# Performance work log

Hardware: AMD Instinct MI355X
Metric: run time of the kernel (lower is better)

## Reference

```python
import jax, jax.numpy as jnp
from jax import lax
import numpy as np

# Straight-through sign (matches SignActivation: >=0 -> +1, <0 -> -1; identity grad)
@jax.custom_vjp
def binarize(x):
    return jnp.where(x >= 0, 1.0, -1.0).astype(x.dtype)

def _bin_fwd(x):
    return binarize(x), None

def _bin_bwd(_, g):
    return (g,)

binarize.defvjp(_bin_fwd, _bin_bwd)

def binary_tanh(x):
    # BinaryTanh: sign(tanh(x) * 2); grad flows through tanh*2 via STE
    return binarize(jnp.tanh(x) * 2)

def conv2d(x, w, b):
    out = lax.conv_general_dilated(x, w, (1, 1), [(1, 1), (1, 1)],
                                   dimension_numbers=('NCHW', 'OIHW', 'NCHW'))
    return out + b[None, :, None, None]

def bn2d(x, g, b, eps=1e-4):
    # training-mode BatchNorm2d: batch stats over (N,H,W), biased variance
    m = jnp.mean(x, axis=(0, 2, 3), keepdims=True)
    v = jnp.mean(jnp.square(x - m), axis=(0, 2, 3), keepdims=True)
    return g[None, :, None, None] * (x - m) * lax.rsqrt(v + eps) + b[None, :, None, None]

def bn1d(x, g, b, eps=1e-5):
    m = jnp.mean(x, axis=0, keepdims=True)
    v = jnp.mean(jnp.square(x - m), axis=0, keepdims=True)
    return g[None, :] * (x - m) * lax.rsqrt(v + eps) + b[None, :]

def maxpool2(x):
    return lax.reduce_window(x, -jnp.inf, lax.max, (1, 1, 2, 2), (1, 1, 2, 2), 'VALID')

def forward(x, w1, b1, g1, be1, w2, b2, g2, be2, w3, b3, g3, be3,
            w4, b4, g4, be4, w5, b5, g5, be5, w6, b6, g6, be6,
            fcw, fcb, g7, be7):
    # block 1 (32x32)
    x = binary_tanh(bn2d(conv2d(x, w1, b1), g1, be1))           # fp conv 3->64
    x = binary_tanh(bn2d(conv2d(x, binarize(w2), b2), g2, be2))  # bin conv 64->64
    x = maxpool2(x)                                              # 16x16
    # block 2
    x = binary_tanh(bn2d(conv2d(x, binarize(w3), b3), g3, be3))  # 64->128
    x = binary_tanh(bn2d(conv2d(x, binarize(w4), b4), g4, be4))  # 128->128
    x = maxpool2(x)                                              # 8x8
    # block 3
    x = binary_tanh(bn2d(conv2d(x, binarize(w5), b5), g5, be5))  # 128->256
    x = binary_tanh(bn2d(conv2d(x, binarize(w6), b6), g6, be6))  # 256->256
    x = maxpool2(x)                                              # 4x4
    x = jnp.mean(x, axis=(2, 3))                                 # AvgPool2d(4) -> [B,256]
    x = x @ binarize(fcw).T + fcb[None, :]                       # BinaryLinear 256->10
    return bn1d(x, g7, be7)

def setup_inputs() -> dict:
    key = jax.random.key(0)
    ks = jax.random.split(key, 32)
    s = 0.05
    d = {
        'x':  jax.random.normal(ks[0], (512, 3, 32, 32), jnp.float32),
        'w1': jax.random.normal(ks[1], (64, 3, 3, 3), jnp.float32) * s,
        'b1': jax.random.normal(ks[2], (64,), jnp.float32) * s,
        'g1': jnp.ones((64,), jnp.float32),  'be1': jnp.zeros((64,), jnp.float32),
        'w2': jax.random.normal(ks[3], (64, 64, 3, 3), jnp.float32) * s,
        'b2': jax.random.normal(ks[4], (64,), jnp.float32) * s,
        'g2': jnp.ones((64,), jnp.float32),  'be2': jnp.zeros((64,), jnp.float32),
        'w3': jax.random.normal(ks[5], (128, 64, 3, 3), jnp.float32) * s,
        'b3': jax.random.normal(ks[6], (128,), jnp.float32) * s,
        'g3': jnp.ones((128,), jnp.float32), 'be3': jnp.zeros((128,), jnp.float32),
        'w4': jax.random.normal(ks[7], (128, 128, 3, 3), jnp.float32) * s,
        'b4': jax.random.normal(ks[8], (128,), jnp.float32) * s,
        'g4': jnp.ones((128,), jnp.float32), 'be4': jnp.zeros((128,), jnp.float32),
        'w5': jax.random.normal(ks[9], (256, 128, 3, 3), jnp.float32) * s,
        'b5': jax.random.normal(ks[10], (256,), jnp.float32) * s,
        'g5': jnp.ones((256,), jnp.float32), 'be5': jnp.zeros((256,), jnp.float32),
        'w6': jax.random.normal(ks[11], (256, 256, 3, 3), jnp.float32) * s,
        'b6': jax.random.normal(ks[12], (256,), jnp.float32) * s,
        'g6': jnp.ones((256,), jnp.float32), 'be6': jnp.zeros((256,), jnp.float32),
        'fcw': jax.random.normal(ks[13], (10, 256), jnp.float32) * s,
        'fcb': jax.random.normal(ks[14], (10,), jnp.float32) * s,
        'g7': jnp.ones((10,), jnp.float32),  'be7': jnp.zeros((10,), jnp.float32),
    }
    return d

def reference(x, w1, b1, g1, be1, w2, b2, g2, be2, w3, b3, g3, be3,
              w4, b4, g4, be4, w5, b5, g5, be5, w6, b6, g6, be6,
              fcw, fcb, g7, be7):
    return forward(x, w1, b1, g1, be1, w2, b2, g2, be2, w3, b3, g3, be3,
                   w4, b4, g4, be4, w5, b5, g5, be5, w6, b6, g6, be6,
                   fcw, fcb, g7, be7)
```

## Files before the change

kernel.cpp:

```cpp
#include <hip/hip_runtime.h>
#include <cstdint>


typedef int v4i __attribute__((ext_vector_type(4)));
typedef int v16i __attribute__((ext_vector_type(16)));

#define NBKT 256
#define SSTR 1664

__global__ void __launch_bounds__(256) pack8(const float* __restrict__ w2,
                                             const float* __restrict__ w3,
                                             const float* __restrict__ w4,
                                             const float* __restrict__ w5,
                                             const float* __restrict__ w6,
                                             int8_t* __restrict__ w8) {
  const int idx = blockIdx.x * 256 + threadIdx.x;
  const float* w; int CiL, e; int8_t* dst;
  if (idx < 36864)        { w = w2; CiL = 64;  e = idx;          dst = w8; }
  else if (idx < 110592)  { w = w3; CiL = 64;  e = idx - 36864;  dst = w8 + 36864; }
  else if (idx < 258048)  { w = w4; CiL = 128; e = idx - 110592; dst = w8 + 110592; }
  else if (idx < 552960)  { w = w5; CiL = 128; e = idx - 258048; dst = w8 + 258048; }
  else if (idx < 1142784) { w = w6; CiL = 256; e = idx - 552960; dst = w8 + 552960; }
  else return;
  const int WDk = CiL / 32;
  const int b = e & 15;
  const int l31 = (e >> 4) & 31;
  const int hi = (e >> 9) & 1;
  const int kc = (e >> 10) % WDk;
  const int tap = (e / (1024 * WDk)) % 9;
  const int cb = e / (9216 * WDk);
  const int co = cb * 32 + l31;
  const int ci = kc * 32 + hi * 16 + b;
  dst[e] = (w[((size_t)co * CiL + ci) * 9 + tap] >= 0.f) ? (int8_t)1 : (int8_t)-1;
}

__global__ void __launch_bounds__(256, 6) conv1_p1(const float* __restrict__ x,
                                                   const float* __restrict__ w1,
                                                   double2* __restrict__ part) {
  __shared__ float ximg[3][34][34];
  __shared__ float wl[16][28];
  __shared__ double pS[16][4], pQ[16][4];
  const int tid = threadIdx.x, n = blockIdx.x, cg = blockIdx.y;
  for (int i = tid; i < 3 * 34 * 34; i += 256) ((float*)ximg)[i] = 0.f;
  for (int i = tid; i < 16 * 27; i += 256) wl[i / 27][i % 27] = w1[cg * 432 + i];
  __syncthreads();
  const float* xb = x + (size_t)n * 3072;
  for (int i = tid; i < 3072; i += 256) {
    const int c = i >> 10, p = i & 1023;
    ximg[c][(p >> 5) + 1][(p & 31) + 1] = xb[i];
  }
  __syncthreads();
  const int h = tid >> 3, w0 = (tid & 7) * 4;
  const int lane = tid & 63, wv = tid >> 6;
  for (int c = 0; c < 16; c += 2) {
    float4 wa4[7], wb4[7];
#pragma unroll
    for (int i = 0; i < 7; i++) {
      wa4[i] = *(const float4*)&wl[c][i * 4];
      wb4[i] = *(const float4*)&wl[c + 1][i * 4];
    }
    const float* wfa = (const float*)wa4;
    const float* wfb = (const float*)wb4;
    float accA[4] = {0.f, 0.f, 0.f, 0.f};
    float accB[4] = {0.f, 0.f, 0.f, 0.f};
#pragma unroll
    for (int ic = 0; ic < 3; ic++)
#pragma unroll
      for (int ky = 0; ky < 3; ky++) {
        float xr[6];
#pragma unroll
        for (int t = 0; t < 6; t++) xr[t] = ximg[ic][h + ky][w0 + t];
#pragma unroll
        for (int kx = 0; kx < 3; kx++) {
          const float wga = wfa[ic * 9 + ky * 3 + kx];
          const float wgb = wfb[ic * 9 + ky * 3 + kx];
#pragma unroll
          for (int j = 0; j < 4; j++) {
            accA[j] = fmaf(xr[j + kx], wga, accA[j]);
            accB[j] = fmaf(xr[j + kx], wgb, accB[j]);
          }
        }
      }
    double s = (double)accA[0] + accA[1] + accA[2] + accA[3];
    double q = (double)accA[0] * accA[0] + (double)accA[1] * accA[1] +
               (double)accA[2] * accA[2] + (double)accA[3] * accA[3];
    double s2 = (double)accB[0] + accB[1] + accB[2] + accB[3];
    double q2 = (double)accB[0] * accB[0] + (double)accB[1] * accB[1] +
                (double)accB[2] * accB[2] + (double)accB[3] * accB[3];
#pragma unroll
    for (int off = 32; off; off >>= 1) {
      s += __shfl_down(s, off);
      q += __shfl_down(q, off);
      s2 += __shfl_down(s2, off);
      q2 += __shfl_down(q2, off);
    }
    if (lane == 0) {
      pS[c][wv] = s;      pQ[c][wv] = q;
      pS[c + 1][wv] = s2; pQ[c + 1][wv] = q2;
    }
  }
  __syncthreads();
  if (tid < 16) {
    const double S = pS[tid][0] + pS[tid][1] + pS[tid][2] + pS[tid][3];
    const double Q = pQ[tid][0] + pQ[tid][1] + pQ[tid][2] + pQ[tid][3];
    part[(size_t)(cg * 16 + tid) * 512 + n] = make_double2(S, Q);
  }
}

__global__ void __launch_bounds__(256) conv1_fin(const double2* __restrict__ part,
                                                 const float* __restrict__ g,
                                                 const float* __restrict__ be,
                                                 const float* __restrict__ w1,
                                                 double2* __restrict__ thr,
                                                 double* __restrict__ te) {
  __shared__ double sS[4], sQ[4];
  const int c = blockIdx.x;
  const int t = threadIdx.x;
  const double2 a = part[(size_t)c * 512 + t];
  const double2 b = part[(size_t)c * 512 + 256 + t];
  double S = a.x + b.x, Q = a.y + b.y;
#pragma unroll
  for (int off = 32; off; off >>= 1) {
    S += __shfl_down(S, off);
    Q += __shfl_down(Q, off);
  }
  if ((t & 63) == 0) { sS[t >> 6] = S; sQ[t >> 6] = Q; }
  __syncthreads();
  if (t != 0) return;
  S = sS[0] + sS[1] + sS[2] + sS[3];
  Q = sQ[0] + sQ[1] + sQ[2] + sQ[3];
  const double Nel = 512.0 * 1024.0;
  const double mu = S / Nel, var = Q / Nel - mu * mu;
  const double r = 1.0 / sqrt(var + 1e-4);
  const double al = (double)g[c] * r;
  const double bt = (double)be[c] - al * mu;
  thr[c] = make_double2(al, bt);
  double ws = 0.0;
  for (int k = 0; k < 27; k++) ws += fabs((double)w1[c * 27 + k]);
  te[c] = fabs(al) * 27.0 * 5.9604644775390625e-08 * ws * 1.25;
}

__global__ void __launch_bounds__(256)
__attribute__((amdgpu_waves_per_eu(2, 2)))
conv1_p2(const float* __restrict__ x, const float* __restrict__ w1,
         const double2* __restrict__ thr, const double* __restrict__ te,
         uint16_t* __restrict__ stg) {
  __shared__ float ximg[3][34][34];
  __shared__ float wl[16][28];
  __shared__ double2 tl[16];
  __shared__ double tel[16];
  __shared__ float smx[4];
  const int tid = threadIdx.x, n = blockIdx.x, cg = blockIdx.y;
  for (int i = tid; i < 3 * 34 * 34; i += 256) ((float*)ximg)[i] = 0.f;
  for (int i = tid; i < 16 * 27; i += 256) wl[i / 27][i % 27] = w1[cg * 432 + i];
  for (int i = tid; i < 16; i += 256) { tl[i] = thr[cg * 16 + i]; tel[i] = te[cg * 16 + i]; }
  __syncthreads();
  const float* xb = x + (size_t)n * 3072;
  float mx = 0.f;
  for (int i = tid; i < 3072; i += 256) {
    const int c = i >> 10, p = i & 1023;
    const float v = xb[i];
    ximg[c][(p >> 5) + 1][(p & 31) + 1] = v;
    mx = fmaxf(mx, fabsf(v));
  }
  const int lane = tid & 63, wv = tid >> 6;
#pragma unroll
  for (int off = 32; off; off >>= 1) mx = fmaxf(mx, __shfl_xor(mx, off));
  if (lane == 0) smx[wv] = mx;
  __syncthreads();
  const double Xmax = (double)fmaxf(fmaxf(smx[0], smx[1]), fmaxf(smx[2], smx[3]));
  const int h = tid >> 3, w0 = (tid & 7) * 4;
  float win[3][3][6];
#pragma unroll
  for (int ic = 0; ic < 3; ic++)
#pragma unroll
    for (int ky = 0; ky < 3; ky++)
#pragma unroll
      for (int t = 0; t < 6; t++) win[ic][ky][t] = ximg[ic][h + ky][w0 + t];
  uint32_t wbits[4] = {0u, 0u, 0u, 0u};
  for (int c = 0; c < 16; c++) {
    float4 wv4[7];
#pragma unroll
    for (int i = 0; i < 7; i++) wv4[i] = *(const float4*)&wl[c][i * 4];
    const float* wf = (const float*)wv4;
    float acc[4] = {0.f, 0.f, 0.f, 0.f};
#pragma unroll
    for (int ic = 0; ic < 3; ic++)
#pragma unroll
      for (int ky = 0; ky < 3; ky++)
#pragma unroll
        for (int kx = 0; kx < 3; kx++) {
          const float wgt = wf[ic * 9 + ky * 3 + kx];
#pragma unroll
          for (int j = 0; j < 4; j++) acc[j] = fmaf(win[ic][ky][j + kx], wgt, acc[j]);
        }
    const double2 ab = tl[c];
    const double ef = tel[c] * Xmax;
#pragma unroll
    for (int j = 0; j < 4; j++) {
      double t = fma(ab.x, (double)acc[j], ab.y);
      if (fabs(t) <= ef) {
        double a64 = 0.0;
        for (int k = 0; k < 27; k++) {
          const int ic = k / 9, rr = k % 9, ky = rr / 3, kx = rr % 3;
          a64 = fma((double)ximg[ic][h + ky][w0 + j + kx], (double)wl[c][k], a64);
        }
        t = fma(ab.x, a64, ab.y);
      }
      if (t >= 0.0) wbits[j] |= 1u << c;
    }
  }
  const int p0 = h * 32 + w0;
  uint2 pkd;
  pkd.x = (wbits[0] & 0xFFFFu) | (wbits[1] << 16);
  pkd.y = (wbits[2] & 0xFFFFu) | (wbits[3] << 16);
  *(uint2*)&stg[(size_t)cg * 524288 + (size_t)n * 1024 + p0] = pkd;
}

__global__ void __launch_bounds__(256) a1merge(const uint16_t* __restrict__ stg,
                                               uint32_t* __restrict__ A1) {
  const int idx = blockIdx.x * 256 + threadIdx.x;
  const int np = idx * 2;
  if (np >= 512 * 1024) return;
  const uint32_t a0 = *(const uint32_t*)&stg[0 * 524288 + np];
  const uint32_t a1 = *(const uint32_t*)&stg[1 * 524288 + np];
  const uint32_t a2 = *(const uint32_t*)&stg[2 * 524288 + np];
  const uint32_t a3 = *(const uint32_t*)&stg[3 * 524288 + np];
  uint4 o;
  o.x = (a0 & 0xFFFFu) | (a1 << 16);
  o.y = (a2 & 0xFFFFu) | (a3 << 16);
  o.z = (a0 >> 16) | (a1 & 0xFFFF0000u);
  o.w = (a2 >> 16) | (a3 & 0xFFFF0000u);
  *(uint4*)&A1[(size_t)np * 2] = o;
}

template <int H, int W, int SH, int Ci, int CO, int WN, int MG, int POOL>
__global__ void __launch_bounds__(256)
__attribute__((amdgpu_waves_per_eu(2, 2)))
mconv(const uint32_t* __restrict__ Ain, const int8_t* __restrict__ w8,
      short* __restrict__ raw, unsigned long long* __restrict__ stats) {
  constexpr int WD = Ci / 32, Wp = W + 2, Cs = Ci + 16, P = H * W;
  constexpr int STRIPS = H / SH;
  constexpr int MT = SH * W / 32;
  constexpr int WM = 4 / WN;
  constexpr int MTW = MT / WM;
  constexpr int NG = MTW / MG;
  constexpr int CHK = 2;
  constexpr int NCH = WD / CHK;
  constexpr int IMGB = (SH + 2) * Wp * Cs;
  constexpr int Wo = W / 2, Po = (H / 2) * Wo;
  static_assert(NG >= 1 && MTW == NG * MG && WD % CHK == 0, "bad geometry");
  __shared__ __align__(16) uint32_t img[IMGB / 4];
  const int tid = threadIdx.x;
  const int n = blockIdx.x / STRIPS, s = blockIdx.x % STRIPS;
  int* __restrict__ mm = (int*)raw;

  for (int i = tid; i < IMGB / 4; i += 256) img[i] = 0u;
  __syncthreads();
  constexpr int ROWW = W * WD;
  for (int i = tid; i < (SH + 2) * ROWW; i += 256) {
    const int lr = i / ROWW;
    const int h = s * SH - 1 + lr;
    if (h < 0 || h >= H) continue;
    const int rem = i % ROWW;
    const int wpx = rem / WD, d = rem % WD;
    const uint32_t bits = Ain[((size_t)n * P + h * W + wpx) * WD + d];
    uint32_t* dst = img + ((lr * Wp + wpx + 1) * Cs) / 4 + d * 8;
#pragma unroll
    for (int nb2 = 0; nb2 < 8; nb2++) {
      const uint32_t t = (((bits >> (4 * nb2)) & 0xFu) * 0x00204081u) & 0x01010101u;
      dst[nb2] = 0x01010101u + (t ^ 0x01010101u) * 0xFEu;
    }
  }
  __syncthreads();

  const int wv = tid >> 6, lane = tid & 63, l31 = lane & 31, hi = lane >> 5;
  const int nb = wv % WN, ms = wv / WN;
  const int cb = blockIdx.y * WN + nb;
  const int co = cb * 32 + l31;
  const int8_t* wbl = w8 + (size_t)cb * 9 * WD * 1024 + (size_t)lane * 16;
  const char* imgb = (const char*)img;
  int sA = 0, qA = 0;
#pragma unroll 1
  for (int mg = 0; mg < NG; mg++) {
    v16i acc[MG];
#pragma unroll
    for (int m = 0; m < MG; m++)
      acc[m] = (v16i){0, 0, 0, 0, 0, 0, 0, 0, 0, 0, 0, 0, 0, 0, 0, 0};
    int ab[MG];
#pragma unroll
    for (int m = 0; m < MG; m++) {
      const int mt = ms * MTW + mg * MG + m;
      const int pp = mt * 32 + l31;
      ab[m] = ((pp / W) * Wp + (pp % W)) * Cs + hi * 16;
    }
#pragma unroll 1
    for (int ch = 0; ch < NCH; ++ch) {
      v4i bf[9 * CHK];
#pragma unroll
      for (int t9 = 0; t9 < 9; t9++)
#pragma unroll
        for (int c = 0; c < CHK; c++)
          bf[t9 * CHK + c] =
              *(const v4i*)(wbl + (size_t)(t9 * WD + ch * CHK + c) * 1024);
#pragma unroll
      for (int tap = 0; tap < 9; tap++) {
        const int toff = ((tap / 3) * Wp + (tap % 3)) * Cs;
#pragma unroll
        for (int c = 0; c < CHK; c++)
#pragma unroll
          for (int m = 0; m < MG; m++) {
            const v4i a =
                *(const v4i*)(imgb + ab[m] + toff + (ch * CHK + c) * 32);
            acc[m] = __builtin_amdgcn_mfma_i32_32x32x32_i8(a, bf[tap * CHK + c],
                                                           acc[m], 0, 0, 0);
          }
      }
    }
#pragma unroll
    for (int m = 0; m < MG; m++)
#pragma unroll
      for (int r = 0; r < 16; r++) {
        const int v = acc[m][r];
        sA += v;
        qA += v * v;
      }
    if constexpr (POOL) {
      if constexpr (W == 32) {
#pragma unroll
        for (int mp = 0; mp < MG / 2; mp++) {
          const int mt0 = ms * MTW + mg * MG + 2 * mp;
          const int ho = (s * SH + mt0) >> 1;
#pragma unroll
          for (int r = 0; r < 16; r += 2) {
            const int v00 = acc[2 * mp][r], v01 = acc[2 * mp][r + 1];
            const int v10 = acc[2 * mp + 1][r], v11 = acc[2 * mp + 1][r + 1];
            const int mn = min(min(v00, v01), min(v10, v11));
            const int mxv = max(max(v00, v01), max(v10, v11));
            const int wo = ((r & 3) + 8 * (r >> 2) + 4 * hi) >> 1;
            mm[((size_t)n * Po + ho * Wo + wo) * CO + co] =
                (int)(((uint32_t)(uint16_t)(short)mxv << 16) |
                      (uint32_t)(uint16_t)(short)mn);
          }
        }
      } else if constexpr (W == 16) {
#pragma unroll
        for (int m = 0; m < MG; m++) {
          const int mt = ms * MTW + mg * MG + m;
          const int ho = (s * SH) / 2 + mt;
#pragma unroll
          for (int r = 0; r < 8; r += 2) {
            const int v00 = acc[m][r], v01 = acc[m][r + 1];
            const int v10 = acc[m][r + 8], v11 = acc[m][r + 9];
            const int mn = min(min(v00, v01), min(v10, v11));
            const int mxv = max(max(v00, v01), max(v10, v11));
            const int wo = ((r & 3) + 8 * (r >> 2) + 4 * hi) >> 1;
            mm[((size_t)n * Po + ho * Wo + wo) * CO + co] =
                (int)(((uint32_t)(uint16_t)(short)mxv << 16) |
                      (uint32_t)(uint16_t)(short)mn);
          }
        }
      } else {
#pragma unroll
        for (int m = 0; m < MG; m++) {
          const int mt = ms * MTW + mg * MG + m;
#pragma unroll
          for (int rb = 0; rb < 2; rb++)
#pragma unroll
            for (int rr = 0; rr < 4; rr += 2) {
              const int r = rb * 8 + rr;
              const int v00 = acc[m][r], v01 = acc[m][r + 1];
              const int v10 = acc[m][r + 4], v11 = acc[m][r + 5];
              const int mn = min(min(v00, v01), min(v10, v11));
              const int mxv = max(max(v00, v01), max(v10, v11));
              const int ho = (s * SH) / 2 + 2 * mt + rb;
              const int wo = (rr + 4 * hi) >> 1;
              mm[((size_t)n * Po + ho * Wo + wo) * CO + co] =
                  (int)(((uint32_t)(uint16_t)(short)mxv << 16) |
                        (uint32_t)(uint16_t)(short)mn);
            }
        }
      }
    } else {
#pragma unroll
      for (int m = 0; m < MG; m++) {
        const int mt = ms * MTW + mg * MG + m;
#pragma unroll
        for (int r = 0; r < 16; r++) {
          const int row = (r & 3) + 8 * (r >> 2) + 4 * hi;
          const int p = s * SH * W + mt * 32 + row;
          raw[((size_t)n * P + p) * CO + co] = (short)acc[m][r];
        }
      }
    }
  }
  sA += __shfl_xor(sA, 32);
  qA += __shfl_xor(qA, 32);
  if (hi == 0) {
    const size_t bkt = (size_t)(blockIdx.x & (NBKT - 1)) * SSTR;
    atomicAdd(&stats[bkt + 2 * co], (unsigned long long)(long long)sA);
    atomicAdd(&stats[bkt + 2 * co + 1], (unsigned long long)(long long)qA);
  }
}

__global__ void __launch_bounds__(256) bin_fin(const unsigned long long* __restrict__ stats,
                                               const float* __restrict__ g,
                                               const float* __restrict__ be,
                                               int2* __restrict__ thri, int Co,
                                               double Nel) {
  __shared__ long long sS[4], sQ[4];
  const int c = blockIdx.x;
  const int t = threadIdx.x;
  long long Si = (long long)stats[(size_t)t * SSTR + 2 * c];
  long long Qi = (long long)stats[(size_t)t * SSTR + 2 * c + 1];
#pragma unroll
  for (int off = 32; off; off >>= 1) {
    Si += __shfl_down(Si, off);
    Qi += __shfl_down(Qi, off);
  }
  if ((t & 63) == 0) { sS[t >> 6] = Si; sQ[t >> 6] = Qi; }
  __syncthreads();
  if (t != 0) return;
  const double S = (double)(sS[0] + sS[1] + sS[2] + sS[3]);
  const double Q = (double)(sQ[0] + sQ[1] + sQ[2] + sQ[3]);
  const double mu = S / Nel, var = Q / Nel - mu * mu;
  const double rr = 1.0 / sqrt(var + 1e-4);
  const double al = (double)g[c] * rr;
  const double bt = (double)be[c] - al * mu;
  int T, dir;
  if (al > 0.0) {
    dir = 1;
    const double tt = -bt / al;
    if (tt >= 6000.0) T = 6000;
    else if (tt <= -6000.0) T = -6000;
    else {
      T = (int)ceil(tt);
      if (fma(al, (double)(T - 1), bt) >= 0.0) T -= 1;
      else if (fma(al, (double)T, bt) < 0.0) T += 1;
    }
  } else if (al < 0.0) {
    dir = 0;
    const double tt = -bt / al;
    if (tt >= 6000.0) T = 6000;
    else if (tt <= -6000.0) T = -6000;
    else {
      T = (int)floor(tt);
      if (fma(al, (double)(T + 1), bt) >= 0.0) T += 1;
      else if (fma(al, (double)T, bt) < 0.0) T -= 1;
    }
  } else {
    dir = 1;
    T = (bt >= 0.0) ? -6000 : 6000;
  }
  thri[c] = make_int2(T, dir);
  (void)Co;
}

template <int P, int CO>
__global__ void __launch_bounds__(256) binz_r(const short* __restrict__ raw,
                                              const int2* __restrict__ thr,
                                              uint32_t* __restrict__ Aout) {
  constexpr int WDo = CO / 32;
  const int idx = blockIdx.x * 256 + threadIdx.x;
  if (idx >= 512 * P * WDo) return;
  const int np = idx / WDo, wd = idx % WDo;
  const short* p = raw + (size_t)np * CO + wd * 32;
  v4i q[4];
#pragma unroll
  for (int t = 0; t < 4; t++) q[t] = __builtin_nontemporal_load((const v4i*)p + t);
  const short* sv = (const short*)q;
  uint32_t word = 0;
#pragma unroll
  for (int j = 0; j < 32; j++) {
    const int v = sv[j];
    const int2 td = thr[wd * 32 + j];
    word |= (uint32_t)(td.y ? (v >= td.x) : (v <= td.x)) << j;
  }
  Aout[idx] = word;
}

template <int Po, int CO>
__global__ void __launch_bounds__(256) binpool_mm(const int* __restrict__ mm,
                                                  const int2* __restrict__ thr,
                                                  uint32_t* __restrict__ Aout) {
  constexpr int WDo = CO / 32;
  const int idx = blockIdx.x * 256 + threadIdx.x;
  if (idx >= 512 * Po * WDo) return;
  const int np = idx / WDo, wd = idx % WDo;
  const int* p = mm + (size_t)np * CO + wd * 32;
  v4i q[8];
#pragma unroll
  for (int t = 0; t < 8; t++) q[t] = __builtin_nontemporal_load((const v4i*)p + t);
  const int* iv = (const int*)q;
  uint32_t word = 0;
#pragma unroll
  for (int j = 0; j < 32; j++) {
    const int v = iv[j];
    const int mn = (short)(v & 0xFFFF), mx = (short)(v >> 16);
    const int2 td = thr[wd * 32 + j];
    const bool b = td.y ? (mx >= td.x) : (mn <= td.x);
    word |= (uint32_t)b << j;
  }
  Aout[idx] = word;
}

__global__ void __launch_bounds__(64) head_kern(const uint32_t* __restrict__ A6,
                                                const float* __restrict__ fcw,
                                                const float* __restrict__ fcb,
                                                float* __restrict__ fcout) {
  __shared__ uint32_t aw[128];
  __shared__ float feat[256];
  const int n = blockIdx.x, t = threadIdx.x;
  for (int i = t; i < 128; i += 64) aw[i] = A6[(size_t)n * 128 + i];
  __syncthreads();
#pragma unroll
  for (int k = 0; k < 4; k++) {
    const int c = t * 4 + k;
    const int wd = c >> 5, sh = c & 31;
    int cnt = 0;
#pragma unroll
    for (int pos = 0; pos < 16; pos++) cnt += (aw[pos * 8 + wd] >> sh) & 1;
    feat[c] = (float)(cnt - 8) * 0.125f;
  }
  __syncthreads();
  if (t < 10) {
    float acc = 0.f;
    for (int c = 0; c < 256; c++) acc += (fcw[t * 256 + c] >= 0.f ? feat[c] : -feat[c]);
    fcout[n * 10 + t] = acc + fcb[t];
  }
}

__global__ void __launch_bounds__(640) bn1d_kern(const float* __restrict__ fcout,
                                                 const float* __restrict__ g7,
                                                 const float* __restrict__ be7,
                                                 float* __restrict__ out) {
  const int t = threadIdx.x, o = t >> 6, lane = t & 63;
  double s = 0.0, q = 0.0;
  float v[8];
#pragma unroll
  for (int i = 0; i < 8; i++) {
    v[i] = fcout[(lane + 64 * i) * 10 + o];
    s += v[i];
    q += (double)v[i] * v[i];
  }
#pragma unroll
  for (int off = 32; off; off >>= 1) {
    s += __shfl_down(s, off);
    q += __shfl_down(q, off);
  }
  s = __shfl(s, 0);
  q = __shfl(q, 0);
  const double mu = s / 512.0, var = q / 512.0 - mu * mu;
  const double r = 1.0 / sqrt(var + 1e-5);
  const double al = (double)g7[o] * r;
  const double bt = (double)be7[o] - al * mu;
#pragma unroll
  for (int i = 0; i < 8; i++) out[(lane + 64 * i) * 10 + o] = (float)fma(al, (double)v[i], bt);
}

extern "C" void kernel_launch(void* const* d_in, const int* in_sizes, int n_in,
                              void* d_out, int out_size, void* d_ws, size_t ws_size,
                              hipStream_t stream) {
  const float* x = (const float*)d_in[0];
  const float* w1 = (const float*)d_in[1];
  const float* g1 = (const float*)d_in[3];
  const float* be1 = (const float*)d_in[4];
  const float* w2 = (const float*)d_in[5];
  const float* g2 = (const float*)d_in[7];
  const float* be2 = (const float*)d_in[8];
  const float* w3 = (const float*)d_in[9];
  const float* g3 = (const float*)d_in[11];
  const float* be3 = (const float*)d_in[12];
  const float* w4 = (const float*)d_in[13];
  const float* g4 = (const float*)d_in[15];
  const float* be4 = (const float*)d_in[16];
  const float* w5 = (const float*)d_in[17];
  const float* g5 = (const float*)d_in[19];
  const float* be5 = (const float*)d_in[20];
  const float* w6 = (const float*)d_in[21];
  const float* g6 = (const float*)d_in[23];
  const float* be6 = (const float*)d_in[24];
  const float* fcw = (const float*)d_in[25];
  const float* fcb = (const float*)d_in[26];
  const float* g7 = (const float*)d_in[27];
  const float* be7 = (const float*)d_in[28];
  float* out = (float*)d_out;

  char* ws = (char*)d_ws;
  size_t off = 0;
  auto take = [&](size_t bytes) -> char* {
    char* p = ws + off;
    off = (off + bytes + 255) & ~(size_t)255;
    return p;
  };
  uint32_t* A1 = (uint32_t*)take((size_t)512 * 1024 * 2 * 4);
  uint32_t* A2 = (uint32_t*)take((size_t)512 * 256 * 2 * 4);
  uint32_t* A3 = (uint32_t*)take((size_t)512 * 256 * 4 * 4);
  uint32_t* A4 = (uint32_t*)take((size_t)512 * 64 * 4 * 4);
  uint32_t* A5 = (uint32_t*)take((size_t)512 * 64 * 8 * 4);
  uint32_t* A6 = (uint32_t*)take((size_t)512 * 16 * 8 * 4);
  int8_t* w8 = (int8_t*)take((size_t)1142784);
  double2* part1 = (double2*)take((size_t)64 * 512 * 16);
  unsigned long long* stats = (unsigned long long*)take((size_t)NBKT * SSTR * 8);
  double2* thrD = (double2*)take((size_t)64 * 16);
  double* teD = (double*)take((size_t)64 * 8);
  int2* thri = (int2*)take((size_t)832 * 8);
  float* fcout = (float*)take((size_t)512 * 10 * 4);
  short* raw = (short*)take((size_t)64 * 512 * 1024 * 2);
  (void)ws_size; (void)in_sizes; (void)n_in; (void)out_size;

  hipMemsetAsync(stats, 0, (size_t)NBKT * SSTR * 8, stream);

  pack8<<<4464, 256, 0, stream>>>(w2, w3, w4, w5, w6, w8);

  conv1_p1<<<dim3(512, 4), 256, 0, stream>>>(x, w1, part1);
  conv1_fin<<<64, 256, 0, stream>>>(part1, g1, be1, w1, thrD, teD);
  conv1_p2<<<dim3(512, 4), 256, 0, stream>>>(x, w1, thrD, teD, (uint16_t*)raw);
  a1merge<<<1024, 256, 0, stream>>>((const uint16_t*)raw, A1);

  mconv<32, 32, 16, 64, 64, 2, 4, 1><<<dim3(1024, 1), 256, 0, stream>>>(A1, w8, raw, stats + 0);
  bin_fin<<<64, 256, 0, stream>>>(stats + 0, g2, be2, thri + 0, 64, 512.0 * 1024.0);
  binpool_mm<256, 64><<<1024, 256, 0, stream>>>((const int*)raw, thri + 0, A2);

  mconv<16, 16, 8, 64, 128, 4, 4, 0><<<dim3(1024, 1), 256, 0, stream>>>(A2, w8 + 36864, raw, stats + 128);
  bin_fin<<<128, 256, 0, stream>>>(stats + 128, g3, be3, thri + 64, 128, 512.0 * 256.0);
  binz_r<256, 128><<<2048, 256, 0, stream>>>(raw, thri + 64, A3);

  mconv<16, 16, 8, 128, 128, 4, 4, 1><<<dim3(1024, 1), 256, 0, stream>>>(A3, w8 + 110592, raw, stats + 384);
  bin_fin<<<128, 256, 0, stream>>>(stats + 384, g4, be4, thri + 192, 128, 512.0 * 256.0);
  binpool_mm<64, 128><<<512, 256, 0, stream>>>((const int*)raw, thri + 192, A4);

  mconv<8, 8, 8, 128, 256, 4, 2, 0><<<dim3(512, 2), 256, 0, stream>>>(A4, w8 + 258048, raw, stats + 640);
  bin_fin<<<256, 256, 0, stream>>>(stats + 640, g5, be5, thri + 320, 256, 512.0 * 64.0);
  binz_r<64, 256><<<1024, 256, 0, stream>>>(raw, thri + 320, A5);

  mconv<8, 8, 8, 256, 256, 4, 2, 1><<<dim3(512, 2), 256, 0, stream>>>(A5, w8 + 552960, raw, stats + 1152);
  bin_fin<<<256, 256, 0, stream>>>(stats + 1152, g6, be6, thri + 576, 256, 512.0 * 64.0);
  binpool_mm<16, 256><<<256, 256, 0, stream>>>((const int*)raw, thri + 576, A6);

  head_kern<<<512, 64, 0, stream>>>(A6, fcw, fcb, fcout);
  bn1d_kern<<<1, 640, 0, stream>>>(fcout, g7, be7, out);
}
```

Baseline: 353.5 us.

## Store conv1 fp32 output in pass 1 and threshold it directly, dropping recompute

Conv1 pass 1 now writes the fp32 convolution results (128 MB) and per-image max |x| to global memory. A new thresholding kernel reads them back, applies the BN sign test with the fp64 fallback near zero, and packs bits straight into A1. This replaces the second conv1 pass and the separate merge kernel. It trades recomputing a cheap 27-tap convolution for a large write plus read of fp32 data, so it may end up limited by memory bandwidth.

New measurement: 668.5 us. 1.89x slower.

```diff
diff --git a/kernel.cpp b/kernel.cpp
--- a/kernel.cpp
+++ b/kernel.cpp
@@ -36,22 +36,34 @@
 
 __global__ void __launch_bounds__(256, 6) conv1_p1(const float* __restrict__ x,
                                                    const float* __restrict__ w1,
-                                                   double2* __restrict__ part) {
+                                                   double2* __restrict__ part,
+                                                   float* __restrict__ convb,
+                                                   float* __restrict__ xmax) {
   __shared__ float ximg[3][34][34];
   __shared__ float wl[16][28];
   __shared__ double pS[16][4], pQ[16][4];
+  __shared__ float smx[4];
   const int tid = threadIdx.x, n = blockIdx.x, cg = blockIdx.y;
   for (int i = tid; i < 3 * 34 * 34; i += 256) ((float*)ximg)[i] = 0.f;
   for (int i = tid; i < 16 * 27; i += 256) wl[i / 27][i % 27] = w1[cg * 432 + i];
   __syncthreads();
   const float* xb = x + (size_t)n * 3072;
+  float mx = 0.f;
   for (int i = tid; i < 3072; i += 256) {
     const int c = i >> 10, p = i & 1023;
-    ximg[c][(p >> 5) + 1][(p & 31) + 1] = xb[i];
-  }
-  __syncthreads();
+    const float v = xb[i];
+    ximg[c][(p >> 5) + 1][(p & 31) + 1] = v;
+    mx = fmaxf(mx, fabsf(v));
+  }
+  const int lane = tid & 63, wv = tid >> 6;
+#pragma unroll
+  for (int off = 32; off; off >>= 1) mx = fmaxf(mx, __shfl_xor(mx, off));
+  if (lane == 0) smx[wv] = mx;
+  __syncthreads();
+  if (cg == 0 && tid == 0)
+    xmax[n] = fmaxf(fmaxf(smx[0], smx[1]), fmaxf(smx[2], smx[3]));
   const int h = tid >> 3, w0 = (tid & 7) * 4;
-  const int lane = tid & 63, wv = tid >> 6;
+  const int p0 = h * 32 + w0;
   for (int c = 0; c < 16; c += 2) {
     float4 wa4[7], wb4[7];
 #pragma unroll
@@ -81,6 +93,10 @@
           }
         }
       }
+    *(float4*)&convb[(size_t)(cg * 16 + c) * 524288 + (size_t)n * 1024 + p0] =
+        make_float4(accA[0], accA[1], accA[2], accA[3]);
+    *(float4*)&convb[(size_t)(cg * 16 + c + 1) * 524288 + (size_t)n * 1024 + p0] =
+        make_float4(accB[0], accB[1], accB[2], accB[3]);
     double s = (double)accA[0] + accA[1] + accA[2] + accA[3];
     double q = (double)accA[0] * accA[0] + (double)accA[1] * accA[1] +
                (double)accA[2] * accA[2] + (double)accA[3] * accA[3];
@@ -140,98 +156,46 @@
   te[c] = fabs(al) * 27.0 * 5.9604644775390625e-08 * ws * 1.25;
 }
 
-__global__ void __launch_bounds__(256)
-__attribute__((amdgpu_waves_per_eu(2, 2)))
-conv1_p2(const float* __restrict__ x, const float* __restrict__ w1,
-         const double2* __restrict__ thr, const double* __restrict__ te,
-         uint16_t* __restrict__ stg) {
-  __shared__ float ximg[3][34][34];
-  __shared__ float wl[16][28];
-  __shared__ double2 tl[16];
-  __shared__ double tel[16];
-  __shared__ float smx[4];
-  const int tid = threadIdx.x, n = blockIdx.x, cg = blockIdx.y;
-  for (int i = tid; i < 3 * 34 * 34; i += 256) ((float*)ximg)[i] = 0.f;
-  for (int i = tid; i < 16 * 27; i += 256) wl[i / 27][i % 27] = w1[cg * 432 + i];
-  for (int i = tid; i < 16; i += 256) { tl[i] = thr[cg * 16 + i]; tel[i] = te[cg * 16 + i]; }
-  __syncthreads();
-  const float* xb = x + (size_t)n * 3072;
-  float mx = 0.f;
-  for (int i = tid; i < 3072; i += 256) {
-    const int c = i >> 10, p = i & 1023;
-    const float v = xb[i];
-    ximg[c][(p >> 5) + 1][(p & 31) + 1] = v;
-    mx = fmaxf(mx, fabsf(v));
-  }
-  const int lane = tid & 63, wv = tid >> 6;
-#pragma unroll
-  for (int off = 32; off; off >>= 1) mx = fmaxf(mx, __shfl_xor(mx, off));
-  if (lane == 0) smx[wv] = mx;
-  __syncthreads();
-  const double Xmax = (double)fmaxf(fmaxf(smx[0], smx[1]), fmaxf(smx[2], smx[3]));
-  const int h = tid >> 3, w0 = (tid & 7) * 4;
-  float win[3][3][6];
-#pragma unroll
-  for (int ic = 0; ic < 3; ic++)
-#pragma unroll
-    for (int ky = 0; ky < 3; ky++)
-#pragma unroll
-      for (int t = 0; t < 6; t++) win[ic][ky][t] = ximg[ic][h + ky][w0 + t];
-  uint32_t wbits[4] = {0u, 0u, 0u, 0u};
-  for (int c = 0; c < 16; c++) {
-    float4 wv4[7];
-#pragma unroll
-    for (int i = 0; i < 7; i++) wv4[i] = *(const float4*)&wl[c][i * 4];
-    const float* wf = (const float*)wv4;
-    float acc[4] = {0.f, 0.f, 0.f, 0.f};
-#pragma unroll
-    for (int ic = 0; ic < 3; ic++)
-#pragma unroll
-      for (int ky = 0; ky < 3; ky++)
-#pragma unroll
-        for (int kx = 0; kx < 3; kx++) {
-          const float wgt = wf[ic * 9 + ky * 3 + kx];
-#pragma unroll
-          for (int j = 0; j < 4; j++) acc[j] = fmaf(win[ic][ky][j + kx], wgt, acc[j]);
-        }
+__global__ void __launch_bounds__(256) thrk(const float* __restrict__ convb,
+                                            const float* __restrict__ x,
+                                            const float* __restrict__ w1,
+                                            const double2* __restrict__ thr,
+                                            const double* __restrict__ te,
+                                            const float* __restrict__ xmax,
+                                            uint32_t* __restrict__ A1) {
+  __shared__ double2 tl[64];
+  __shared__ double tel[64];
+  const int tid = threadIdx.x;
+  if (tid < 64) { tl[tid] = thr[tid]; tel[tid] = te[tid]; }
+  __syncthreads();
+  const int np = blockIdx.x * 256 + tid;
+  const int n = np >> 10, p = np & 1023;
+  const double Xm = (double)xmax[n];
+  uint32_t b0 = 0, b1 = 0;
+#pragma unroll 4
+  for (int c = 0; c < 64; c++) {
+    const float v = convb[(size_t)c * 524288 + np];
     const double2 ab = tl[c];
-    const double ef = tel[c] * Xmax;
-#pragma unroll
-    for (int j = 0; j < 4; j++) {
-      double t = fma(ab.x, (double)acc[j], ab.y);
-      if (fabs(t) <= ef) {
-        double a64 = 0.0;
-        for (int k = 0; k < 27; k++) {
-          const int ic = k / 9, rr = k % 9, ky = rr / 3, kx = rr % 3;
-          a64 = fma((double)ximg[ic][h + ky][w0 + j + kx], (double)wl[c][k], a64);
-        }
-        t = fma(ab.x, a64, ab.y);
+    double t = fma(ab.x, (double)v, ab.y);
+    if (fabs(t) <= tel[c] * Xm) {
+      const int h = p >> 5, w = p & 31;
+      double a64 = 0.0;
+      for (int k = 0; k < 27; k++) {
+        const int ic = k / 9, rr = k % 9, ky = rr / 3, kx = rr % 3;
+        const int hh = h + ky - 1, ww = w + kx - 1;
+        double xv = 0.0;
+        if (hh >= 0 && hh < 32 && ww >= 0 && ww < 32)
+          xv = (double)x[(size_t)n * 3072 + ic * 1024 + hh * 32 + ww];
+        a64 = fma(xv, (double)w1[c * 27 + k], a64);
       }
-      if (t >= 0.0) wbits[j] |= 1u << c;
-    }
-  }
-  const int p0 = h * 32 + w0;
-  uint2 pkd;
-  pkd.x = (wbits[0] & 0xFFFFu) | (wbits[1] << 16);
-  pkd.y = (wbits[2] & 0xFFFFu) | (wbits[3] << 16);
-  *(uint2*)&stg[(size_t)cg * 524288 + (size_t)n * 1024 + p0] = pkd;
-}
-
-__global__ void __launch_bounds__(256) a1merge(const uint16_t* __restrict__ stg,
-                                               uint32_t* __restrict__ A1) {
-  const int idx = blockIdx.x * 256 + threadIdx.x;
-  const int np = idx * 2;
-  if (np >= 512 * 1024) return;
-  const uint32_t a0 = *(const uint32_t*)&stg[0 * 524288 + np];
-  const uint32_t a1 = *(const uint32_t*)&stg[1 * 524288 + np];
-  const uint32_t a2 = *(const uint32_t*)&stg[2 * 524288 + np];
-  const uint32_t a3 = *(const uint32_t*)&stg[3 * 524288 + np];
-  uint4 o;
-  o.x = (a0 & 0xFFFFu) | (a1 << 16);
-  o.y = (a2 & 0xFFFFu) | (a3 << 16);
-  o.z = (a0 >> 16) | (a1 & 0xFFFF0000u);
-  o.w = (a2 >> 16) | (a3 & 0xFFFF0000u);
-  *(uint4*)&A1[(size_t)np * 2] = o;
+      t = fma(ab.x, a64, ab.y);
+    }
+    if (t >= 0.0) {
+      if (c < 32) b0 |= 1u << c;
+      else b1 |= 1u << (c - 32);
+    }
+  }
+  *(uint2*)&A1[(size_t)np * 2] = make_uint2(b0, b1);
 }
 
 template <int H, int W, int SH, int Ci, int CO, int WN, int MG, int POOL>
@@ -606,17 +570,18 @@
   double* teD = (double*)take((size_t)64 * 8);
   int2* thri = (int2*)take((size_t)832 * 8);
   float* fcout = (float*)take((size_t)512 * 10 * 4);
-  short* raw = (short*)take((size_t)64 * 512 * 1024 * 2);
+  float* xmaxb = (float*)take((size_t)512 * 4);
+  float* convb = (float*)take((size_t)64 * 524288 * 4);
+  short* raw = (short*)convb;
   (void)ws_size; (void)in_sizes; (void)n_in; (void)out_size;
 
   hipMemsetAsync(stats, 0, (size_t)NBKT * SSTR * 8, stream);
 
   pack8<<<4464, 256, 0, stream>>>(w2, w3, w4, w5, w6, w8);
 
-  conv1_p1<<<dim3(512, 4), 256, 0, stream>>>(x, w1, part1);
+  conv1_p1<<<dim3(512, 4), 256, 0, stream>>>(x, w1, part1, convb, xmaxb);
   conv1_fin<<<64, 256, 0, stream>>>(part1, g1, be1, w1, thrD, teD);
-  conv1_p2<<<dim3(512, 4), 256, 0, stream>>>(x, w1, thrD, teD, (uint16_t*)raw);
-  a1merge<<<1024, 256, 0, stream>>>((const uint16_t*)raw, A1);
+  thrk<<<2048, 256, 0, stream>>>(convb, x, w1, thrD, teD, xmaxb, A1);
 
   mconv<32, 32, 16, 64, 64, 2, 4, 1><<<dim3(1024, 1), 256, 0, stream>>>(A1, w8, raw, stats + 0);
   bin_fin<<<64, 256, 0, stream>>>(stats + 0, g2, be2, thri + 0, 64, 512.0 * 1024.0);
```
